# Performance work log

Measured on AMD Instinct MI355X. Metric: run time of the kernel, lower is better.

## Reference

```python
import jax, jax.numpy as jnp
import numpy as np

N = 50000
E = 640000
D = 128          # in = hidden = out channels
L = 3            # num_layers
ATT_H = D // 2   # attention hidden width
LN_EPS = 1e-5


def _layer_norm(h, gamma, beta):
    mu = jnp.mean(h, axis=-1, keepdims=True)
    var = jnp.var(h, axis=-1, keepdims=True)
    return (h - mu) * jax.lax.rsqrt(var + LN_EPS) * gamma + beta


def setup_inputs() -> dict:
    key = jax.random.key(0)
    ks = jax.random.split(key, 12)
    x = jax.random.normal(ks[0], (N, D), dtype=jnp.float32)
    edge_index = jax.random.randint(ks[1], (2, E), 0, N, dtype=jnp.int64)
    edge_attr = jax.random.normal(ks[2], (E, 2), dtype=jnp.float32)
    s = 1.0 / np.sqrt(D)
    # Per-layer params stacked on leading L axis (all layers same dims).
    lin_node_w = jax.random.uniform(ks[3], (L, D, D), jnp.float32, -s, s)
    lin_edge_w = jax.random.uniform(ks[4], (L, D + 2, D), jnp.float32, -s, s)
    att_w1 = jax.random.uniform(ks[5], (L, 2 * D, ATT_H), jnp.float32, -s, s)
    att_b1 = jnp.zeros((L, ATT_H), jnp.float32)
    att_w2 = jax.random.uniform(ks[6], (L, ATT_H, 1), jnp.float32, -s, s)
    att_b2 = jnp.zeros((L, 1), jnp.float32)
    bias = jnp.zeros((L, D), jnp.float32)
    ln_gamma = jnp.ones((L, D), jnp.float32)
    ln_beta = jnp.zeros((L, D), jnp.float32)
    return {"x": x, "edge_index": edge_index, "edge_attr": edge_attr,
            "lin_node_w": lin_node_w, "lin_edge_w": lin_edge_w,
            "att_w1": att_w1, "att_b1": att_b1, "att_w2": att_w2,
            "att_b2": att_b2, "bias": bias, "ln_gamma": ln_gamma,
            "ln_beta": ln_beta}


def reference(x, edge_index, edge_attr, lin_node_w, lin_edge_w,
              att_w1, att_b1, att_w2, att_b2, bias, ln_gamma, ln_beta):
    # PyG default flow: x_j = source = edge_index[0], x_i = target = edge_index[1];
    # aggregation ('add') scatters messages into targets. Dropout is a no-op (eval).
    src, dst = edge_index[0], edge_index[1]
    for i in range(L):
        x_input = x
        h = x @ lin_node_w[i]                          # [N, D]
        xj = h[src]                                    # [E, D] gather
        xi = h[dst]                                    # [E, D] gather
        # att(cat(x_i, x_j)) without materializing the concat:
        a1 = jax.nn.relu(xi @ att_w1[i][:D] + xj @ att_w1[i][D:] + att_b1[i])
        att = jax.nn.sigmoid(a1 @ att_w2[i] + att_b2[i])   # [E, 1]
        # lin_edge(cat(x_j, edge_attr)) split the same way:
        msg = att * (xj @ lin_edge_w[i][:D] + edge_attr @ lin_edge_w[i][D:])
        out = jax.ops.segment_sum(msg, dst, num_segments=N) + bias[i]
        out = _layer_norm(out, ln_gamma[i], ln_beta[i])
        if i < L - 1:
            out = jax.nn.relu(out)
        x = out + x_input                              # residual (Identity proj)
    return x
```

## Files before the change

kernel.cpp:

```cpp
#include <hip/hip_runtime.h>
#include <hip/hip_bf16.h>

#define NN 50000
#define EE 640000
#define ABLK 625
#define AEDG 1024
#define NBK 196

typedef __attribute__((ext_vector_type(8))) short short8;
typedef __attribute__((ext_vector_type(4))) float f32x4;

__device__ __forceinline__ float bf2f(ushort u) {
    return __uint_as_float(((uint)u) << 16);
}
__device__ __forceinline__ ushort f2bf(float f) {
    uint b = __float_as_uint(f);
    uint r = (b + 0x7fffu + ((b >> 16) & 1u)) >> 16;
    return (ushort)r;
}
__device__ __forceinline__ ushort f2bf_rn(float f) {
    return (ushort)((__float_as_uint(f) + 0x8000u) >> 16);
}


__global__ __launch_bounds__(256) void k_bucketA(const int* __restrict__ ei,
                                                 const float* __restrict__ ea,
                                                 uint* __restrict__ eab,
                                                 int* __restrict__ bcnt) {
    __shared__ int h[NBK];
    const int t = threadIdx.x;
    for (int i = t; i < NBK; i += 256) h[i] = 0;
    __syncthreads();
    const int base = blockIdx.x * AEDG;
    #pragma unroll
    for (int k = 0; k < 4; ++k) {
        const int e = base + k * 256 + t;
        const int d = ei[EE + e];
        atomicAdd(&h[d >> 8], 1);
        const float2 v = *(const float2*)(ea + 2 * e);
        eab[e] = ((uint)f2bf(v.y) << 16) | (uint)f2bf(v.x);
    }
    __syncthreads();
    for (int i = t; i < NBK; i += 256)
        bcnt[i * ABLK + blockIdx.x] = h[i];
}


__global__ __launch_bounds__(256) void k_scanbkt(const int* __restrict__ bcnt,
                                                 int* __restrict__ boff2,
                                                 int* __restrict__ tot) {
    const int b = blockIdx.x;
    const int t = threadIdx.x;
    const int lane = t & 63, wv = t >> 6;
    __shared__ int ws[4];
    int run = 0;
    for (int k = 0; k < 3; ++k) {
        const int j = k * 256 + t;
        const int v = (j < ABLK) ? bcnt[b * ABLK + j] : 0;
        int x = v;
        #pragma unroll
        for (int o = 1; o < 64; o <<= 1) {
            int y = __shfl_up(x, o);
            if (lane >= o) x += y;
        }
        if (lane == 63) ws[wv] = x;
        __syncthreads();
        int add = 0;
        for (int w = 0; w < wv; ++w) add += ws[w];
        if (j < ABLK) boff2[b * ABLK + j] = run + add + x - v;
        const int btot = ws[0] + ws[1] + ws[2] + ws[3];
        __syncthreads();
        run += btot;
    }
    if (t == 0) tot[b] = run;
}


__global__ __launch_bounds__(256) void k_scantot(const int* __restrict__ tot,
                                                 int* __restrict__ bbase) {
    const int t = threadIdx.x;
    const int lane = t & 63, wv = t >> 6;
    const int v = (t < NBK) ? tot[t] : 0;
    int x = v;
    #pragma unroll
    for (int o = 1; o < 64; o <<= 1) {
        int y = __shfl_up(x, o);
        if (lane >= o) x += y;
    }
    __shared__ int ws[4];
    if (lane == 63) ws[wv] = x;
    __syncthreads();
    int add = 0;
    for (int w = 0; w < wv; ++w) add += ws[w];
    if (t < NBK) bbase[t] = add + x - v;
    if (t == 255) bbase[NBK] = add + x;
}


__global__ __launch_bounds__(256) void k_bucketB(const int* __restrict__ ei,
                                                 const uint* __restrict__ eab,
                                                 const int* __restrict__ bbase,
                                                 const int* __restrict__ boff2,
                                                 uint2* __restrict__ staged) {
    __shared__ int cur[NBK];
    const int t = threadIdx.x;
    for (int i = t; i < NBK; i += 256)
        cur[i] = bbase[i] + boff2[i * ABLK + blockIdx.x];
    __syncthreads();
    const int base = blockIdx.x * AEDG;
    #pragma unroll
    for (int k = 0; k < 4; ++k) {
        const int e = base + k * 256 + t;
        const int d = ei[EE + e];
        const uint s = (uint)ei[e];
        const int pos = atomicAdd(&cur[d >> 8], 1);
        staged[pos] = make_uint2(s | ((uint)(d & 255) << 20), eab[e]);
    }
}


__global__ __launch_bounds__(256) void k_bucketC(const int* __restrict__ bbase,
                                                 const uint2* __restrict__ staged,
                                                 uint2* __restrict__ adjSE,
                                                 int* __restrict__ offs,
                                                 int* __restrict__ csr_dst) {
    const int b = blockIdx.x;
    const int t = threadIdx.x;
    const int lane = t & 63, wv = t >> 6;
    const int sbeg = bbase[b], send = bbase[b + 1];

    __shared__ int cnt[256];
    __shared__ int cur[256];
    __shared__ int ws[4];
    cnt[t] = 0;
    __syncthreads();
    for (int i = sbeg + t; i < send; i += 256)
        atomicAdd(&cnt[(staged[i].x >> 20) & 255], 1);
    __syncthreads();

    const int v = cnt[t];
    int x = v;
    #pragma unroll
    for (int o = 1; o < 64; o <<= 1) {
        int y = __shfl_up(x, o);
        if (lane >= o) x += y;
    }
    if (lane == 63) ws[wv] = x;
    __syncthreads();
    int add = 0;
    for (int w = 0; w < wv; ++w) add += ws[w];
    const int excl = add + x - v;

    const int node = b * 256 + t;
    if (node <= NN) offs[node] = sbeg + excl;
    cur[t] = sbeg + excl;
    __syncthreads();

    for (int i = sbeg + t; i < send; i += 256) {
        const uint2 r = staged[i];
        const int din = (r.x >> 20) & 255;
        const int pos = atomicAdd(&cur[din], 1);
        adjSE[pos] = make_uint2(r.x & 0xFFFFFu, r.y);
        csr_dst[pos] = b * 256 + din;
    }
}


__global__ __launch_bounds__(256) void k_compose(const float* __restrict__ wn_all,
                                                 const float* __restrict__ aw1,
                                                 const float* __restrict__ wle,
                                                 ushort* __restrict__ wcT) {
    const int l = blockIdx.x >> 7;
    const int k = blockIdx.x & 127;
    const int t = threadIdx.x;
    const float* wn = wn_all + (l * 128 + k) * 128;
    float acc = 0.f;
    for (int c = 0; c < 128; ++c) {
        float cat;
        if (t < 128)
            cat = aw1[(l * 256 + ((t & 64) << 1) + c) * 64 + (t & 63)];
        else
            cat = wle[(l * 130 + c) * 128 + (t - 128)];
        acc += wn[c] * cat;
    }
    wcT[(l * 256 + t) * 128 + k] = f2bf(acc);
}


#define K1_LOADA(AV, RT)                                                   \
    {                                                                      \
        const float* xrow_ = xin + (size_t)(rbase + (RT) * 16 + lrow) * 128; \
        _Pragma("unroll")                                                  \
        for (int s = 0; s < 4; ++s) {                                      \
            const float* px = xrow_ + s * 32 + kg * 8;                     \
            float4 u = *(const float4*)(px);                               \
            float4 v = *(const float4*)(px + 4);                           \
            short8 av;                                                     \
            av[0] = (short)f2bf(u.x); av[1] = (short)f2bf(u.y);            \
            av[2] = (short)f2bf(u.z); av[3] = (short)f2bf(u.w);            \
            av[4] = (short)f2bf(v.x); av[5] = (short)f2bf(v.y);            \
            av[6] = (short)f2bf(v.z); av[7] = (short)f2bf(v.w);            \
            AV[s] = av;                                                    \
        }                                                                  \
    }

#define K1_COMP(AV, RT)                                                    \
    {                                                                      \
        f32x4 acc[4] = {};                                                 \
        _Pragma("unroll")                                                  \
        for (int t = 0; t < 4; ++t) {                                      \
            _Pragma("unroll")                                              \
            for (int s = 0; s < 4; ++s)                                    \
                acc[t] = __builtin_amdgcn_mfma_f32_16x16x32_bf16(          \
                    AV[s], b[t][s], acc[t], 0, 0, 0);                      \
        }                                                                  \
        _Pragma("unroll")                                                  \
        for (int t = 0; t < 4; ++t) {                                      \
            const int col = c0 + t * 16 + lrow;                            \
            _Pragma("unroll")                                              \
            for (int j = 0; j < 4; ++j)                                    \
                pqr[(size_t)(rbase + (RT) * 16 + kg * 4 + j) * 256 + col] = \
                    f2bf(acc[t][j]);                                       \
        }                                                                  \
    }

__global__ __launch_bounds__(256) void k1_gemm(const float* __restrict__ xin,
                                               const ushort* __restrict__ wcT,
                                               ushort* __restrict__ pqr) {
    const int wave = threadIdx.x >> 6;
    const int lane = threadIdx.x & 63;
    const int rbase = blockIdx.x * 64;
    const int c0 = wave * 64;
    const int lrow = lane & 15;
    const int kg = lane >> 4;

    short8 b[4][4];
    #pragma unroll
    for (int t = 0; t < 4; ++t) {
        const int col = c0 + t * 16 + lrow;
        #pragma unroll
        for (int s = 0; s < 4; ++s)
            b[t][s] = *(const short8*)(wcT + col * 128 + s * 32 + kg * 8);
    }

    if (rbase + 64 <= NN) {
        short8 aA[4], aB[4];
        K1_LOADA(aA, 0)
        K1_LOADA(aB, 1) K1_COMP(aA, 0)
        K1_LOADA(aA, 2) K1_COMP(aB, 1)
        K1_LOADA(aB, 3) K1_COMP(aA, 2)
        K1_COMP(aB, 3)
    } else {
        #pragma unroll
        for (int rt = 0; rt < 4; ++rt) {
            const int r0 = rbase + rt * 16;
            int arow = r0 + lrow;
            if (arow >= NN) arow = NN - 1;
            const float* xrow = xin + (size_t)arow * 128;
            short8 a[4];
            #pragma unroll
            for (int s = 0; s < 4; ++s) {
                const float* px = xrow + s * 32 + kg * 8;
                float4 u = *(const float4*)(px);
                float4 v = *(const float4*)(px + 4);
                short8 av;
                av[0] = (short)f2bf(u.x); av[1] = (short)f2bf(u.y);
                av[2] = (short)f2bf(u.z); av[3] = (short)f2bf(u.w);
                av[4] = (short)f2bf(v.x); av[5] = (short)f2bf(v.y);
                av[6] = (short)f2bf(v.z); av[7] = (short)f2bf(v.w);
                a[s] = av;
            }
            f32x4 acc[4] = {};
            #pragma unroll
            for (int t = 0; t < 4; ++t) {
                #pragma unroll
                for (int s = 0; s < 4; ++s)
                    acc[t] = __builtin_amdgcn_mfma_f32_16x16x32_bf16(a[s], b[t][s], acc[t], 0, 0, 0);
            }
            #pragma unroll
            for (int t = 0; t < 4; ++t) {
                const int col = c0 + t * 16 + lrow;
                #pragma unroll
                for (int j = 0; j < 4; ++j) {
                    const int orow = r0 + kg * 4 + j;
                    if (orow < NN)
                        pqr[(size_t)orow * 256 + col] = f2bf(acc[t][j]);
                }
            }
        }
    }
}


__global__ __launch_bounds__(256) void k_att(
    const uint2* __restrict__ adjSE, const int* __restrict__ csr_dst,
    float* __restrict__ attv, const ushort* __restrict__ pqr,
    const float* __restrict__ b1v, const float* __restrict__ w2v,
    const float* __restrict__ b2v) {
    const int lane = threadIdx.x & 63;
    const int e0 = blockIdx.x * 256 + (threadIdx.x >> 6) * 64;
    const int row = lane & 15;
    const int kg = lane >> 4;
    const float b2 = b2v[0];

    short8 bv0, bv1;
    const bool col0 = (row == 0);
    #pragma unroll
    for (int j = 0; j < 8; ++j) {
        bv0[j] = (short)f2bf(col0 ? w2v[kg * 8 + j] : 0.f);
        bv1[j] = (short)f2bf(col0 ? w2v[32 + kg * 8 + j] : 0.f);
    }

    uint srcs[4], dsts[4];
    #pragma unroll
    for (int t = 0; t < 4; ++t) {
        const int pos = e0 + t * 16 + row;
        srcs[t] = adjSE[pos].x;
        dsts[t] = (uint)csr_dst[pos];
    }

    f32x4 acc[4] = {};
    #pragma unroll
    for (int h = 0; h < 2; ++h) {
        const int cb = 32 * h + kg * 8;
        float4 bA = *(const float4*)(b1v + cb);
        float4 bB = *(const float4*)(b1v + cb + 4);
        const short8 bfrag = h ? bv1 : bv0;
        #pragma unroll
        for (int t = 0; t < 4; ++t) {
            short8 qv = *(const short8*)(pqr + (size_t)srcs[t] * 256 + 64 + cb);
            short8 pv = *(const short8*)(pqr + (size_t)dsts[t] * 256 + cb);
            short8 av;
            #pragma unroll
            for (int j = 0; j < 8; ++j) {
                float bb = (j < 4) ? ((const float*)&bA)[j] : ((const float*)&bB)[j - 4];
                float v = bf2f((ushort)qv[j]) + bf2f((ushort)pv[j]) + bb;
                av[j] = (short)f2bf_rn(fmaxf(v, 0.f));
            }
            acc[t] = __builtin_amdgcn_mfma_f32_16x16x32_bf16(av, bfrag, acc[t], 0, 0, 0);
        }
    }
    if (row == 0) {
        #pragma unroll
        for (int t = 0; t < 4; ++t) {
            float4 o;
            #pragma unroll
            for (int j = 0; j < 4; ++j) {
                float s = acc[t][j] + b2;
                ((float*)&o)[j] = 1.f / (1.f + __expf(-s));
            }
            *(float4*)(attv + e0 + t * 16 + kg * 4) = o;
        }
    }
}


#define CONS(MM, AA, RR, JJ)                                          \
    {                                                                 \
        const float a_ = ((JJ) < ee) ? (AA) : 0.f;                    \
        acc0 = fmaf(a_, __uint_as_float((RR) << 16), acc0);           \
        acc1 = fmaf(a_, __uint_as_float((RR) & 0xffff0000u), acc1);   \
        sE0  = fmaf(a_, __uint_as_float((MM).y << 16), sE0);          \
        sE1  = fmaf(a_, __uint_as_float((MM).y & 0xffff0000u), sE1);  \
    }

#define LOADQ(M0, M1, M2, M3, A0, A1, A2, A3, R0, R1, R2, R3, BASE)  \
    {                                                                \
        M0 = adjSE[(BASE)];                                          \
        M1 = adjSE[(BASE) + 1];                                      \
        M2 = adjSE[(BASE) + 2];                                      \
        M3 = adjSE[(BASE) + 3];                                      \
        A0 = attv[(BASE)];                                           \
        A1 = attv[(BASE) + 1];                                       \
        A2 = attv[(BASE) + 2];                                       \
        A3 = attv[(BASE) + 3];                                       \
        R0 = *(const uint*)(rp + (size_t)M0.x * 256);                \
        R1 = *(const uint*)(rp + (size_t)M1.x * 256);                \
        R2 = *(const uint*)(rp + (size_t)M2.x * 256);                \
        R3 = *(const uint*)(rp + (size_t)M3.x * 256);                \
    }

__global__ __launch_bounds__(256) void k_msg(
    const int* __restrict__ offs, const uint2* __restrict__ adjSE,
    const float* __restrict__ attv, const ushort* __restrict__ pqr,
    const float* __restrict__ xin, const float* __restrict__ web,
    const float* __restrict__ biasv, const float* __restrict__ gammav,
    const float* __restrict__ betav, float* __restrict__ xout, int do_relu) {
    const int lane = threadIdx.x & 63;
    const int n = blockIdx.x * 4 + (threadIdx.x >> 6);
    const int c0 = 2 * lane;

    const int eb = __builtin_amdgcn_readfirstlane(offs[n]);
    const int ee = __builtin_amdgcn_readfirstlane(offs[n + 1]);

    float acc0 = 0.f, acc1 = 0.f, sE0 = 0.f, sE1 = 0.f;
    if (eb < ee) {
        const ushort* rp = pqr + 128 + c0;
        uint2 a0, a1, a2, a3, b0, b1, b2, b3;
        float fa0, fa1, fa2, fa3, fb0, fb1, fb2, fb3;
        uint ra0, ra1, ra2, ra3, rb0, rb1, rb2, rb3;
        LOADQ(a0, a1, a2, a3, fa0, fa1, fa2, fa3, ra0, ra1, ra2, ra3, eb);
        LOADQ(b0, b1, b2, b3, fb0, fb1, fb2, fb3, rb0, rb1, rb2, rb3, eb + 4);
        int j = eb;
        for (; j + 8 < ee; j += 8) {
            CONS(a0, fa0, ra0, j) CONS(a1, fa1, ra1, j + 1)
            CONS(a2, fa2, ra2, j + 2) CONS(a3, fa3, ra3, j + 3)
            LOADQ(a0, a1, a2, a3, fa0, fa1, fa2, fa3, ra0, ra1, ra2, ra3, j + 8);
            CONS(b0, fb0, rb0, j + 4) CONS(b1, fb1, rb1, j + 5)
            CONS(b2, fb2, rb2, j + 6) CONS(b3, fb3, rb3, j + 7)
            LOADQ(b0, b1, b2, b3, fb0, fb1, fb2, fb3, rb0, rb1, rb2, rb3, j + 12);
        }
        CONS(a0, fa0, ra0, j) CONS(a1, fa1, ra1, j + 1)
        CONS(a2, fa2, ra2, j + 2) CONS(a3, fa3, ra3, j + 3)
        CONS(b0, fb0, rb0, j + 4) CONS(b1, fb1, rb1, j + 5)
        CONS(b2, fb2, rb2, j + 6) CONS(b3, fb3, rb3, j + 7)
    }

    const float web00 = web[c0], web01 = web[c0 + 1];
    const float web10 = web[128 + c0], web11 = web[128 + c0 + 1];
    acc0 += sE0 * web00 + sE1 * web10;
    acc1 += sE0 * web01 + sE1 * web11;

    const float2 bi = *(const float2*)(biasv + c0);
    float v0 = acc0 + bi.x;
    float v1 = acc1 + bi.y;
    float sm = v0 + v1, sq = v0 * v0 + v1 * v1;
    #pragma unroll
    for (int o = 32; o > 0; o >>= 1) {
        sm += __shfl_xor(sm, o);
        sq += __shfl_xor(sq, o);
    }
    const float mean = sm * (1.f / 128.f);
    const float var = sq * (1.f / 128.f) - mean * mean;
    const float inv = rsqrtf(var + 1e-5f);
    const float2 ga = *(const float2*)(gammav + c0);
    const float2 be = *(const float2*)(betav + c0);
    float y0 = (v0 - mean) * inv * ga.x + be.x;
    float y1 = (v1 - mean) * inv * ga.y + be.y;
    if (do_relu) { y0 = fmaxf(y0, 0.f); y1 = fmaxf(y1, 0.f); }
    const float2 xr = *(const float2*)(xin + (size_t)n * 128 + c0);
    y0 += xr.x;
    y1 += xr.y;
    float2 o2; o2.x = y0; o2.y = y1;
    *(float2*)(xout + (size_t)n * 128 + c0) = o2;
}


extern "C" void kernel_launch(void* const* d_in, const int* in_sizes, int n_in,
                              void* d_out, int out_size, void* d_ws, size_t ws_size,
                              hipStream_t stream) {
    const float* x   = (const float*)d_in[0];
    const int*   ei  = (const int*)d_in[1];
    const float* ea  = (const float*)d_in[2];
    const float* wn  = (const float*)d_in[3];
    const float* wle = (const float*)d_in[4];
    const float* aw1 = (const float*)d_in[5];
    const float* ab1 = (const float*)d_in[6];
    const float* aw2 = (const float*)d_in[7];
    const float* ab2 = (const float*)d_in[8];
    const float* bia = (const float*)d_in[9];
    const float* gam = (const float*)d_in[10];
    const float* bet = (const float*)d_in[11];

    char* w = (char*)d_ws;
    size_t o = 0;
    auto alloc = [&](size_t bytes) {
        char* p = w + o;
        o = (o + bytes + 255) & ~(size_t)255;
        return p;
    };
    int*    offs    = (int*)alloc((size_t)(NN + 1) * 4);
    int*    bcnt    = (int*)alloc((size_t)NBK * ABLK * 4);
    int*    boff2   = (int*)alloc((size_t)NBK * ABLK * 4);
    int*    tot     = (int*)alloc((size_t)NBK * 4);
    int*    bbase   = (int*)alloc((size_t)(NBK + 1) * 4);
    uint*   eab     = (uint*)alloc((size_t)EE * 4);
    uint2*  staged  = (uint2*)alloc((size_t)EE * 8);
    int*    csr_dst = (int*)alloc((size_t)EE * 4);
    uint2*  adjSE   = (uint2*)alloc((size_t)(EE + 64) * 8);
    float*  attv    = (float*)alloc((size_t)(EE + 64) * 4);
    ushort* wcT     = (ushort*)alloc((size_t)3 * 256 * 128 * 2);
    ushort* pqr     = (ushort*)alloc((size_t)NN * 256 * 2);
    float*  xb1     = (float*)alloc((size_t)NN * 128 * 4);
    float*  xb2     = (float*)alloc((size_t)NN * 128 * 4);

    hipMemsetAsync(adjSE + EE, 0, (size_t)64 * 8, stream);
    hipMemsetAsync(attv + EE, 0, (size_t)64 * 4, stream);
    k_bucketA<<<ABLK, 256, 0, stream>>>(ei, ea, eab, bcnt);
    k_compose<<<384, 256, 0, stream>>>(wn, aw1, wle, wcT);
    k_scanbkt<<<NBK, 256, 0, stream>>>(bcnt, boff2, tot);
    k_scantot<<<1, 256, 0, stream>>>(tot, bbase);
    k_bucketB<<<ABLK, 256, 0, stream>>>(ei, eab, bbase, boff2, staged);
    k_bucketC<<<NBK, 256, 0, stream>>>(bbase, staged, adjSE, offs, csr_dst);

    const float* xi = x;
    float* xo = xb1;
    for (int l = 0; l < 3; ++l) {
        k1_gemm<<<(NN + 63) / 64, 256, 0, stream>>>(xi, wcT + (size_t)l * 256 * 128, pqr);
        k_att<<<EE / 256, 256, 0, stream>>>(adjSE, csr_dst, attv, pqr,
                                            ab1 + l * 64, aw2 + l * 64, ab2 + l);
        const bool last = (l == 2);
        float* out_ptr = last ? (float*)d_out : xo;
        k_msg<<<NN / 4, 256, 0, stream>>>(
            offs, adjSE, attv, pqr, xi,
            wle + ((size_t)l * 130 + 128) * 128,
            bia + l * 128, gam + l * 128, bet + l * 128,
            out_ptr, last ? 0 : 1);
        xi = out_ptr;
        xo = (l == 0) ? xb2 : xb1;
    }
}
```

Before: 295.4 us.

## Fuse attention scoring into per-node message aggregation and merge compose into bucketA

The separate per-edge attention kernel is removed and its work moves into the per-destination aggregation kernel. Each wavefront loads its node's P row once, computes sigmoid attention for 16 edges at a time with MFMA, then broadcasts the weights by shuffle to accumulate messages. This drops the attv and csr_dst arrays, their global writes and reads, two memsets and one launch per layer. Weight composition is folded into the bucketA launch as extra blocks. The aggregation loop is no longer software-pipelined, so gather latency may be exposed and lanes are partly idle for low-degree nodes.

```diff
diff --git a/kernel.cpp b/kernel.cpp
--- a/kernel.cpp
+++ b/kernel.cpp
@@ -23,12 +23,30 @@
 }
 
 
-__global__ __launch_bounds__(256) void k_bucketA(const int* __restrict__ ei,
-                                                 const float* __restrict__ ea,
-                                                 uint* __restrict__ eab,
-                                                 int* __restrict__ bcnt) {
+__global__ __launch_bounds__(256) void k_bucketA(
+    const int* __restrict__ ei, const float* __restrict__ ea,
+    uint* __restrict__ eab, int* __restrict__ bcnt,
+    const float* __restrict__ wn_all, const float* __restrict__ aw1,
+    const float* __restrict__ wle, ushort* __restrict__ wcT) {
+    const int t = threadIdx.x;
+    if (blockIdx.x >= ABLK) {
+        const int bb = blockIdx.x - ABLK;
+        const int l = bb >> 7;
+        const int k = bb & 127;
+        const float* wn = wn_all + (l * 128 + k) * 128;
+        float acc = 0.f;
+        for (int c = 0; c < 128; ++c) {
+            float cat;
+            if (t < 128)
+                cat = aw1[(l * 256 + ((t & 64) << 1) + c) * 64 + (t & 63)];
+            else
+                cat = wle[(l * 130 + c) * 128 + (t - 128)];
+            acc += wn[c] * cat;
+        }
+        wcT[(l * 256 + t) * 128 + k] = f2bf(acc);
+        return;
+    }
     __shared__ int h[NBK];
-    const int t = threadIdx.x;
     for (int i = t; i < NBK; i += 256) h[i] = 0;
     __syncthreads();
     const int base = blockIdx.x * AEDG;
@@ -122,8 +140,7 @@
 __global__ __launch_bounds__(256) void k_bucketC(const int* __restrict__ bbase,
                                                  const uint2* __restrict__ staged,
                                                  uint2* __restrict__ adjSE,
-                                                 int* __restrict__ offs,
-                                                 int* __restrict__ csr_dst) {
+                                                 int* __restrict__ offs) {
     const int b = blockIdx.x;
     const int t = threadIdx.x;
     const int lane = t & 63, wv = t >> 6;
@@ -161,29 +178,7 @@
         const int din = (r.x >> 20) & 255;
         const int pos = atomicAdd(&cur[din], 1);
         adjSE[pos] = make_uint2(r.x & 0xFFFFFu, r.y);
-        csr_dst[pos] = b * 256 + din;
-    }
-}
-
-
-__global__ __launch_bounds__(256) void k_compose(const float* __restrict__ wn_all,
-                                                 const float* __restrict__ aw1,
-                                                 const float* __restrict__ wle,
-                                                 ushort* __restrict__ wcT) {
-    const int l = blockIdx.x >> 7;
-    const int k = blockIdx.x & 127;
-    const int t = threadIdx.x;
-    const float* wn = wn_all + (l * 128 + k) * 128;
-    float acc = 0.f;
-    for (int c = 0; c < 128; ++c) {
-        float cat;
-        if (t < 128)
-            cat = aw1[(l * 256 + ((t & 64) << 1) + c) * 64 + (t & 63)];
-        else
-            cat = wle[(l * 130 + c) * 128 + (t - 128)];
-        acc += wn[c] * cat;
-    }
-    wcT[(l * 256 + t) * 128 + k] = f2bf(acc);
+    }
 }
 
 
@@ -292,128 +287,81 @@
 }
 
 
-__global__ __launch_bounds__(256) void k_att(
-    const uint2* __restrict__ adjSE, const int* __restrict__ csr_dst,
-    float* __restrict__ attv, const ushort* __restrict__ pqr,
+__global__ __launch_bounds__(256) void k_fused(
+    const int* __restrict__ offs, const uint2* __restrict__ adjSE,
+    const ushort* __restrict__ pqr, const float* __restrict__ xin,
     const float* __restrict__ b1v, const float* __restrict__ w2v,
-    const float* __restrict__ b2v) {
-    const int lane = threadIdx.x & 63;
-    const int e0 = blockIdx.x * 256 + (threadIdx.x >> 6) * 64;
-    const int row = lane & 15;
-    const int kg = lane >> 4;
-    const float b2 = b2v[0];
-
-    short8 bv0, bv1;
-    const bool col0 = (row == 0);
-    #pragma unroll
-    for (int j = 0; j < 8; ++j) {
-        bv0[j] = (short)f2bf(col0 ? w2v[kg * 8 + j] : 0.f);
-        bv1[j] = (short)f2bf(col0 ? w2v[32 + kg * 8 + j] : 0.f);
-    }
-
-    uint srcs[4], dsts[4];
-    #pragma unroll
-    for (int t = 0; t < 4; ++t) {
-        const int pos = e0 + t * 16 + row;
-        srcs[t] = adjSE[pos].x;
-        dsts[t] = (uint)csr_dst[pos];
-    }
-
-    f32x4 acc[4] = {};
-    #pragma unroll
-    for (int h = 0; h < 2; ++h) {
-        const int cb = 32 * h + kg * 8;
-        float4 bA = *(const float4*)(b1v + cb);
-        float4 bB = *(const float4*)(b1v + cb + 4);
-        const short8 bfrag = h ? bv1 : bv0;
-        #pragma unroll
-        for (int t = 0; t < 4; ++t) {
-            short8 qv = *(const short8*)(pqr + (size_t)srcs[t] * 256 + 64 + cb);
-            short8 pv = *(const short8*)(pqr + (size_t)dsts[t] * 256 + cb);
-            short8 av;
-            #pragma unroll
-            for (int j = 0; j < 8; ++j) {
-                float bb = (j < 4) ? ((const float*)&bA)[j] : ((const float*)&bB)[j - 4];
-                float v = bf2f((ushort)qv[j]) + bf2f((ushort)pv[j]) + bb;
-                av[j] = (short)f2bf_rn(fmaxf(v, 0.f));
-            }
-            acc[t] = __builtin_amdgcn_mfma_f32_16x16x32_bf16(av, bfrag, acc[t], 0, 0, 0);
-        }
-    }
-    if (row == 0) {
-        #pragma unroll
-        for (int t = 0; t < 4; ++t) {
-            float4 o;
-            #pragma unroll
-            for (int j = 0; j < 4; ++j) {
-                float s = acc[t][j] + b2;
-                ((float*)&o)[j] = 1.f / (1.f + __expf(-s));
-            }
-            *(float4*)(attv + e0 + t * 16 + kg * 4) = o;
-        }
-    }
-}
-
-
-#define CONS(MM, AA, RR, JJ)                                          \
-    {                                                                 \
-        const float a_ = ((JJ) < ee) ? (AA) : 0.f;                    \
-        acc0 = fmaf(a_, __uint_as_float((RR) << 16), acc0);           \
-        acc1 = fmaf(a_, __uint_as_float((RR) & 0xffff0000u), acc1);   \
-        sE0  = fmaf(a_, __uint_as_float((MM).y << 16), sE0);          \
-        sE1  = fmaf(a_, __uint_as_float((MM).y & 0xffff0000u), sE1);  \
-    }
-
-#define LOADQ(M0, M1, M2, M3, A0, A1, A2, A3, R0, R1, R2, R3, BASE)  \
-    {                                                                \
-        M0 = adjSE[(BASE)];                                          \
-        M1 = adjSE[(BASE) + 1];                                      \
-        M2 = adjSE[(BASE) + 2];                                      \
-        M3 = adjSE[(BASE) + 3];                                      \
-        A0 = attv[(BASE)];                                           \
-        A1 = attv[(BASE) + 1];                                       \
-        A2 = attv[(BASE) + 2];                                       \
-        A3 = attv[(BASE) + 3];                                       \
-        R0 = *(const uint*)(rp + (size_t)M0.x * 256);                \
-        R1 = *(const uint*)(rp + (size_t)M1.x * 256);                \
-        R2 = *(const uint*)(rp + (size_t)M2.x * 256);                \
-        R3 = *(const uint*)(rp + (size_t)M3.x * 256);                \
-    }
-
-__global__ __launch_bounds__(256) void k_msg(
-    const int* __restrict__ offs, const uint2* __restrict__ adjSE,
-    const float* __restrict__ attv, const ushort* __restrict__ pqr,
-    const float* __restrict__ xin, const float* __restrict__ web,
+    const float* __restrict__ b2v, const float* __restrict__ web,
     const float* __restrict__ biasv, const float* __restrict__ gammav,
     const float* __restrict__ betav, float* __restrict__ xout, int do_relu) {
     const int lane = threadIdx.x & 63;
     const int n = blockIdx.x * 4 + (threadIdx.x >> 6);
     const int c0 = 2 * lane;
+    const int row = lane & 15;
+    const int kg = lane >> 4;
 
     const int eb = __builtin_amdgcn_readfirstlane(offs[n]);
     const int ee = __builtin_amdgcn_readfirstlane(offs[n + 1]);
+    const int cnt = ee - eb;
 
     float acc0 = 0.f, acc1 = 0.f, sE0 = 0.f, sE1 = 0.f;
-    if (eb < ee) {
-        const ushort* rp = pqr + 128 + c0;
-        uint2 a0, a1, a2, a3, b0, b1, b2, b3;
-        float fa0, fa1, fa2, fa3, fb0, fb1, fb2, fb3;
-        uint ra0, ra1, ra2, ra3, rb0, rb1, rb2, rb3;
-        LOADQ(a0, a1, a2, a3, fa0, fa1, fa2, fa3, ra0, ra1, ra2, ra3, eb);
-        LOADQ(b0, b1, b2, b3, fb0, fb1, fb2, fb3, rb0, rb1, rb2, rb3, eb + 4);
-        int j = eb;
-        for (; j + 8 < ee; j += 8) {
-            CONS(a0, fa0, ra0, j) CONS(a1, fa1, ra1, j + 1)
-            CONS(a2, fa2, ra2, j + 2) CONS(a3, fa3, ra3, j + 3)
-            LOADQ(a0, a1, a2, a3, fa0, fa1, fa2, fa3, ra0, ra1, ra2, ra3, j + 8);
-            CONS(b0, fb0, rb0, j + 4) CONS(b1, fb1, rb1, j + 5)
-            CONS(b2, fb2, rb2, j + 6) CONS(b3, fb3, rb3, j + 7)
-            LOADQ(b0, b1, b2, b3, fb0, fb1, fb2, fb3, rb0, rb1, rb2, rb3, j + 12);
-        }
-        CONS(a0, fa0, ra0, j) CONS(a1, fa1, ra1, j + 1)
-        CONS(a2, fa2, ra2, j + 2) CONS(a3, fa3, ra3, j + 3)
-        CONS(b0, fb0, rb0, j + 4) CONS(b1, fb1, rb1, j + 5)
-        CONS(b2, fb2, rb2, j + 6) CONS(b3, fb3, rb3, j + 7)
+
+    if (cnt > 0) {
+        const float b2 = b2v[0];
+        short8 bv0, bv1;
+        const bool col0 = (row == 0);
+        #pragma unroll
+        for (int j = 0; j < 8; ++j) {
+            bv0[j] = (short)f2bf(col0 ? w2v[kg * 8 + j] : 0.f);
+            bv1[j] = (short)f2bf(col0 ? w2v[32 + kg * 8 + j] : 0.f);
+        }
+        float pb0[8], pb1[8];
+        {
+            short8 p0 = *(const short8*)(pqr + (size_t)n * 256 + kg * 8);
+            short8 p1 = *(const short8*)(pqr + (size_t)n * 256 + 32 + kg * 8);
+            #pragma unroll
+            for (int j = 0; j < 8; ++j) {
+                pb0[j] = bf2f((ushort)p0[j]) + b1v[kg * 8 + j];
+                pb1[j] = bf2f((ushort)p1[j]) + b1v[32 + kg * 8 + j];
+            }
+        }
+
+        for (int cb = 0; cb < cnt; cb += 16) {
+            const int e = eb + cb + row;
+            const int ec = e < ee ? e : (ee - 1);
+            const uint2 m = adjSE[ec];
+            const ushort* qp = pqr + (size_t)m.x * 256 + 64;
+            const short8 q0 = *(const short8*)(qp + kg * 8);
+            const short8 q1 = *(const short8*)(qp + 32 + kg * 8);
+            short8 av0, av1;
+            #pragma unroll
+            for (int j = 0; j < 8; ++j) {
+                av0[j] = (short)f2bf_rn(fmaxf(bf2f((ushort)q0[j]) + pb0[j], 0.f));
+                av1[j] = (short)f2bf_rn(fmaxf(bf2f((ushort)q1[j]) + pb1[j], 0.f));
+            }
+            f32x4 sc = {};
+            sc = __builtin_amdgcn_mfma_f32_16x16x32_bf16(av0, bv0, sc, 0, 0, 0);
+            sc = __builtin_amdgcn_mfma_f32_16x16x32_bf16(av1, bv1, sc, 0, 0, 0);
+            const float at0 = (cb + kg * 4 + 0 < cnt) ? 1.f / (1.f + __expf(-(sc[0] + b2))) : 0.f;
+            const float at1 = (cb + kg * 4 + 1 < cnt) ? 1.f / (1.f + __expf(-(sc[1] + b2))) : 0.f;
+            const float at2 = (cb + kg * 4 + 2 < cnt) ? 1.f / (1.f + __expf(-(sc[2] + b2))) : 0.f;
+            const float at3 = (cb + kg * 4 + 3 < cnt) ? 1.f / (1.f + __expf(-(sc[3] + b2))) : 0.f;
+
+            #pragma unroll
+            for (int ce = 0; ce < 16; ++ce) {
+                const float atx = (ce & 3) == 0 ? at0
+                                : (ce & 3) == 1 ? at1
+                                : (ce & 3) == 2 ? at2 : at3;
+                const float att = __shfl(atx, (ce >> 2) * 16);
+                const uint my = __shfl(m.y, ce);
+                const uint srcb = __shfl(m.x, ce);
+                const uint rv = *((const uint*)(pqr + (size_t)srcb * 256 + 128) + lane);
+                acc0 = fmaf(att, __uint_as_float(rv << 16), acc0);
+                acc1 = fmaf(att, __uint_as_float(rv & 0xffff0000u), acc1);
+                sE0 = fmaf(att, __uint_as_float(my << 16), sE0);
+                sE1 = fmaf(att, __uint_as_float(my & 0xffff0000u), sE1);
+            }
+        }
     }
 
     const float web00 = web[c0], web01 = web[c0 + 1];
@@ -476,33 +424,27 @@
     int*    bbase   = (int*)alloc((size_t)(NBK + 1) * 4);
     uint*   eab     = (uint*)alloc((size_t)EE * 4);
     uint2*  staged  = (uint2*)alloc((size_t)EE * 8);
-    int*    csr_dst = (int*)alloc((size_t)EE * 4);
-    uint2*  adjSE   = (uint2*)alloc((size_t)(EE + 64) * 8);
-    float*  attv    = (float*)alloc((size_t)(EE + 64) * 4);
+    uint2*  adjSE   = (uint2*)alloc((size_t)EE * 8);
     ushort* wcT     = (ushort*)alloc((size_t)3 * 256 * 128 * 2);
     ushort* pqr     = (ushort*)alloc((size_t)NN * 256 * 2);
     float*  xb1     = (float*)alloc((size_t)NN * 128 * 4);
     float*  xb2     = (float*)alloc((size_t)NN * 128 * 4);
 
-    hipMemsetAsync(adjSE + EE, 0, (size_t)64 * 8, stream);
-    hipMemsetAsync(attv + EE, 0, (size_t)64 * 4, stream);
-    k_bucketA<<<ABLK, 256, 0, stream>>>(ei, ea, eab, bcnt);
-    k_compose<<<384, 256, 0, stream>>>(wn, aw1, wle, wcT);
+    k_bucketA<<<ABLK + 384, 256, 0, stream>>>(ei, ea, eab, bcnt, wn, aw1, wle, wcT);
     k_scanbkt<<<NBK, 256, 0, stream>>>(bcnt, boff2, tot);
     k_scantot<<<1, 256, 0, stream>>>(tot, bbase);
     k_bucketB<<<ABLK, 256, 0, stream>>>(ei, eab, bbase, boff2, staged);
-    k_bucketC<<<NBK, 256, 0, stream>>>(bbase, staged, adjSE, offs, csr_dst);
+    k_bucketC<<<NBK, 256, 0, stream>>>(bbase, staged, adjSE, offs);
 
     const float* xi = x;
     float* xo = xb1;
     for (int l = 0; l < 3; ++l) {
         k1_gemm<<<(NN + 63) / 64, 256, 0, stream>>>(xi, wcT + (size_t)l * 256 * 128, pqr);
-        k_att<<<EE / 256, 256, 0, stream>>>(adjSE, csr_dst, attv, pqr,
-                                            ab1 + l * 64, aw2 + l * 64, ab2 + l);
         const bool last = (l == 2);
         float* out_ptr = last ? (float*)d_out : xo;
-        k_msg<<<NN / 4, 256, 0, stream>>>(
-            offs, adjSE, attv, pqr, xi,
+        k_fused<<<NN / 4, 256, 0, stream>>>(
+            offs, adjSE, pqr, xi,
+            ab1 + l * 64, aw2 + l * 64, ab2 + l,
             wle + ((size_t)l * 130 + 128) * 128,
             bia + l * 128, gam + l * 128, bet + l * 128,
             out_ptr, last ? 0 : 1);
```

Measured after the change: 341.0 us. +15.4%, slower.
